# Kernel tuning notes

Hardware: AMD Instinct MI355X
Metric: run time of the kernel (lower is better)

The kernel has to match this reference:

```python
import jax, jax.numpy as jnp
import numpy as np

B, T = 64, 512
V, E, H, L = 100000, 256, 256, 9


def _lstm(x, Wx, Wh, b):
    # x: [B,T,E] -> hs: [B,T,H]; Keras gate order i,f,c,o
    xg = jnp.einsum('bte,eg->btg', x, Wx) + b  # [B,T,4H]
    h0 = jnp.zeros((x.shape[0], Wh.shape[0]), x.dtype)

    def step(carry, xt):
        h, c = carry
        g = xt + h @ Wh
        i, f, gc, o = jnp.split(g, 4, axis=-1)
        c = jax.nn.sigmoid(f) * c + jax.nn.sigmoid(i) * jnp.tanh(gc)
        h = jax.nn.sigmoid(o) * jnp.tanh(c)
        return (h, c), h

    _, hs = jax.lax.scan(step, (h0, h0), jnp.swapaxes(xg, 0, 1))
    return jnp.swapaxes(hs, 0, 1)


def _crf_log_likelihood(logits, tags, seq_len, trans):
    # logits: [B,T,L], tags: [B,T] int, seq_len: [B] int, trans: [L,L]
    Bb, Tt, Ll = logits.shape
    t_idx = jnp.arange(Tt)
    mask = (t_idx[None, :] < seq_len[:, None]).astype(logits.dtype)  # [B,T]
    # gold path score: unary + pairwise transitions
    unary = jnp.take_along_axis(logits, tags[..., None], axis=-1)[..., 0]  # [B,T]
    unary_score = jnp.sum(unary * mask, axis=-1)
    binary = trans[tags[:, :-1], tags[:, 1:]]  # [B,T-1]
    binary_score = jnp.sum(binary * mask[:, 1:], axis=-1)
    score = unary_score + binary_score
    # forward algorithm (log partition)
    alpha0 = logits[:, 0]  # [B,L]
    step_mask = t_idx[1:, None] < seq_len[None, :]  # [T-1,B]

    def step(alpha, xs):
        logit_t, m = xs  # [B,L], [B]
        new = jax.nn.logsumexp(alpha[:, :, None] + trans[None], axis=1) + logit_t
        alpha = jnp.where(m[:, None], new, alpha)
        return alpha, None

    alpha, _ = jax.lax.scan(step, alpha0, (jnp.swapaxes(logits[:, 1:], 0, 1), step_mask))
    log_norm = jax.nn.logsumexp(alpha, axis=-1)  # [B]
    return score - log_norm


def setup_inputs() -> dict:
    key = jax.random.key(0)
    ks = jax.random.split(key, 12)
    s = 0.05
    return {
        'tokens': jax.random.randint(ks[0], (B, T), 0, V),
        'labels': jax.random.randint(ks[1], (B, T), 0, L),
        'emb_table': jax.random.normal(ks[2], (V, E), jnp.float32) * s,
        'Wx_f': jax.random.normal(ks[3], (E, 4 * H), jnp.float32) * s,
        'Wh_f': jax.random.normal(ks[4], (H, 4 * H), jnp.float32) * s,
        'b_f': jnp.zeros((4 * H,), jnp.float32),
        'Wx_b': jax.random.normal(ks[5], (E, 4 * H), jnp.float32) * s,
        'Wh_b': jax.random.normal(ks[6], (H, 4 * H), jnp.float32) * s,
        'b_b': jnp.zeros((4 * H,), jnp.float32),
        'W_dense': jax.random.normal(ks[7], (2 * H, L), jnp.float32) * s,
        'b_dense': jnp.zeros((L,), jnp.float32),
        'trans': jax.random.uniform(ks[8], (L, L), jnp.float32),
    }


def reference(tokens, labels, emb_table, Wx_f, Wh_f, b_f, Wx_b, Wh_b, b_b, W_dense, b_dense, trans):
    # seq_len = count of non-pad (nonzero) tokens, as in the original call()
    seq_len = jnp.sum((tokens != 0).astype(jnp.int32), axis=-1)  # [B]
    emb = emb_table[tokens]  # [B,T,E]  (dropout inactive at inference)
    h_fwd = _lstm(emb, Wx_f, Wh_f, b_f)
    h_bwd = _lstm(emb[:, ::-1], Wx_b, Wh_b, b_b)[:, ::-1]
    enc = jnp.concatenate([h_fwd, h_bwd], axis=-1)  # [B,T,2H]
    logits = enc @ W_dense + b_dense  # [B,T,L]
    ll = _crf_log_likelihood(logits, labels, seq_len, trans)  # [B]
    return logits, seq_len, ll
```

## Files before the change

### kernel.cpp

```cpp
#include <hip/hip_runtime.h>
#include <hip/hip_fp16.h>


typedef unsigned int  uint32;
typedef unsigned short ushort16;
typedef unsigned long long uint64;
typedef __attribute__((ext_vector_type(8))) short  short8;
typedef __attribute__((ext_vector_type(4))) float  floatx4;
typedef __attribute__((ext_vector_type(2))) _Float16 half2t;

#define BB 64
#define TT 512
#define NT (BB*TT)
#define G4 1024
#define NL 9

__device__ inline float bf2f(ushort16 u) {
  return __builtin_bit_cast(float, ((uint32)u) << 16);
}
__device__ inline ushort16 f2bf(float f) {
  uint32 u = __builtin_bit_cast(uint32, f);
  u += 0x7fffu + ((u >> 16) & 1u);
  return (ushort16)(u >> 16);
}
__device__ inline float sigf(float x)  { return 1.0f / (1.0f + __expf(-x)); }
__device__ inline float tanhf_(float x){ return 1.0f - 2.0f / (1.0f + __expf(2.0f * x)); }

__device__ inline float fdot2_(uint32 w, half2t h, float acc) {
  return __builtin_amdgcn_fdot2(__builtin_bit_cast(half2t, w), h, acc, false);
}

__device__ inline void bar_lds() {
  __builtin_amdgcn_sched_barrier(0);
  asm volatile("s_waitcnt lgkmcnt(0)" ::: "memory");
  __builtin_amdgcn_s_barrier();
  __builtin_amdgcn_sched_barrier(0);
}

__global__ __launch_bounds__(64) void k_seqlen(const int* __restrict__ tokens,
                                               int* __restrict__ slen,
                                               float* __restrict__ out_sl) {
  const int b = blockIdx.x, lane = threadIdx.x;
  int cnt = 0;
  for (int t = lane; t < TT; t += 64) cnt += (tokens[b * TT + t] != 0) ? 1 : 0;
  #pragma unroll
  for (int off = 32; off >= 1; off >>= 1) cnt += __shfl_down(cnt, off, 64);
  if (lane == 0) { slen[b] = cnt; out_sl[b] = (float)cnt; }
}

__global__ __launch_bounds__(256) void k_embed(const int* __restrict__ tokens,
                                               const float* __restrict__ emb,
                                               ushort16* __restrict__ A) {
  const int f = blockIdx.x * 256 + threadIdx.x;
  const int e = f * 4;
  const int row = e >> 8;
  const int col = e & 255;
  const int tok = tokens[row];
  const float4 v = *(const float4*)(emb + (size_t)tok * 256 + col);
  uint32 lo = (uint32)f2bf(v.x) | ((uint32)f2bf(v.y) << 16);
  uint32 hi = (uint32)f2bf(v.z) | ((uint32)f2bf(v.w) << 16);
  *(uint2*)(A + e) = make_uint2(lo, hi);
}

__global__ __launch_bounds__(256) void k_wxprep(const float* __restrict__ Wxf,
                                                const float* __restrict__ Wxb,
                                                ushort16* __restrict__ BT) {
  const int id = blockIdx.x * 256 + threadIdx.x;
  const int c = id >> 8, k = id & 255;
  const float v = (c < G4) ? Wxf[k * G4 + c] : Wxb[k * G4 + (c - G4)];
  BT[c * 256 + k] = f2bf(v);
}

__global__ __launch_bounds__(256) void k_whprep(const float* __restrict__ Wh,
                                                uint32* __restrict__ W2) {
  const int id = blockIdx.x * 256 + threadIdx.x;
  const int k2 = id >> 10, c = id & 1023;
  const float w0 = Wh[(2 * k2) * G4 + c];
  const float w1 = Wh[(2 * k2 + 1) * G4 + c];
  const ushort16 b0 = __builtin_bit_cast(ushort16, (_Float16)w0);
  const ushort16 b1 = __builtin_bit_cast(ushort16, (_Float16)w1);
  W2[id] = ((uint32)b1 << 16) | (uint32)b0;
}

__global__ __launch_bounds__(256) void k_gemm_xg(const ushort16* __restrict__ A,
                                                 const ushort16* __restrict__ BT,
                                                 const float* __restrict__ bias_f,
                                                 const float* __restrict__ bias_b,
                                                 ushort16* __restrict__ xgf,
                                                 ushort16* __restrict__ xgb) {
  __shared__ __align__(16) ushort16 As[64 * 36];
  __shared__ __align__(16) ushort16 Bs[64 * 36];
  const int m0 = blockIdx.x * 64;
  const int n0 = blockIdx.y * 64;
  const int tid = threadIdx.x;
  const int wave = tid >> 6, lane = tid & 63;
  const int lr = tid >> 2;
  const int lc = (tid & 3) * 8;
  const int am = lane & 15, aq = lane >> 4;
  floatx4 acc[4];
  #pragma unroll
  for (int j = 0; j < 4; ++j) acc[j] = (floatx4){0.f, 0.f, 0.f, 0.f};

  for (int k0 = 0; k0 < 256; k0 += 32) {
    const uint4 va = *(const uint4*)(A  + ((m0 + lr) * 256 + k0 + lc));
    const uint4 vb = *(const uint4*)(BT + ((n0 + lr) * 256 + k0 + lc));
    *(uint2*)&As[lr * 36 + lc]     = make_uint2(va.x, va.y);
    *(uint2*)&As[lr * 36 + lc + 4] = make_uint2(va.z, va.w);
    *(uint2*)&Bs[lr * 36 + lc]     = make_uint2(vb.x, vb.y);
    *(uint2*)&Bs[lr * 36 + lc + 4] = make_uint2(vb.z, vb.w);
    __syncthreads();
    union { uint2 u[2]; short8 s; } fa, fb;
    fa.u[0] = *(const uint2*)&As[(wave * 16 + am) * 36 + aq * 8];
    fa.u[1] = *(const uint2*)&As[(wave * 16 + am) * 36 + aq * 8 + 4];
    #pragma unroll
    for (int j = 0; j < 4; ++j) {
      fb.u[0] = *(const uint2*)&Bs[(j * 16 + am) * 36 + aq * 8];
      fb.u[1] = *(const uint2*)&Bs[(j * 16 + am) * 36 + aq * 8 + 4];
      acc[j] = __builtin_amdgcn_mfma_f32_16x16x32_bf16(fa.s, fb.s, acc[j], 0, 0, 0);
    }
    __syncthreads();
  }
  const int orow = m0 + wave * 16 + aq * 4;
  #pragma unroll
  for (int j = 0; j < 4; ++j) {
    const int col = n0 + j * 16 + am;
    const float bv = (col < G4) ? bias_f[col] : bias_b[col - G4];
    #pragma unroll
    for (int r = 0; r < 4; ++r) {
      const float v = acc[j][r] + bv;
      const int row = orow + r;
      if (col < G4) xgf[row * G4 + col] = f2bf(v);
      else          xgb[row * G4 + (col - G4)] = f2bf(v);
    }
  }
}

__global__ __launch_bounds__(256) void k_zero(uint64* __restrict__ xh) {
  xh[blockIdx.x * 256 + threadIdx.x] = 0ull;
}

__global__ __launch_bounds__(1024, 1) void k_lstm(const ushort16* __restrict__ xgf,
                                                  const ushort16* __restrict__ xgb,
                                                  const uint32* __restrict__ Whf,
                                                  const uint32* __restrict__ Whb,
                                                  uint64* __restrict__ xh,
                                                  float* __restrict__ enc) {
  __shared__ __align__(16) uint32 h2[2][128];
  __shared__ float gl[512];
  __shared__ float glp[512];
  const int bid  = blockIdx.x;
  const int dir  = bid >> 7;
  const int b    = (bid >> 1) & 63;
  const int half = bid & 1;
  const int tid  = threadIdx.x;
  const int l    = tid & 63;
  const int c512 = tid & 511;
  const int q = c512 >> 7, r = c512 & 127;
  const int col = q * 256 + half * 128 + r;
  const bool ownk = (tid < 512);
  const ushort16* __restrict__ xg = dir ? xgb : xgf;
  const uint32* __restrict__ W2   = dir ? Whb : Whf;
  uint64* const xmine = xh + ((size_t)bid << 7);
  const uint64* const xpeer = xh + ((size_t)(bid ^ 1) << 7);

  const int rowbase = ownk ? (half * 64) : (64 - half * 64);
  uint32 wv[64];
  #pragma unroll
  for (int i = 0; i < 64; ++i) wv[i] = W2[(rowbase + i) * 1024 + col];
  #pragma unroll
  for (int i = 0; i < 64; ++i) asm volatile("" : "+v"(wv[i]));

  if (tid < 128) h2[0][tid] = 0u;
  float c_state = 0.f;
  __syncthreads();

  ushort16 xA = (ushort16)0;
  if (ownk) {
    const int t0 = dir ? (TT - 1) : 0;
    xA = xg[(size_t)(b * TT + t0) * G4 + col];
  }

#define HC(u) __builtin_bit_cast(half2t, u)
#define GR4(B,W) { const uint4 hq = hb[B]; \
                 a0 = fdot2_(wv[(W)*4+0], HC(hq.x), a0); \
                 a1 = fdot2_(wv[(W)*4+1], HC(hq.y), a1); \
                 a2 = fdot2_(wv[(W)*4+2], HC(hq.z), a2); \
                 a3 = fdot2_(wv[(W)*4+3], HC(hq.w), a3); }

  for (int s = 0; s < TT; ++s) {
    const int par = s & 1;
    float a0 = 0.f, a1 = 0.f, a2 = 0.f, a3 = 0.f;
    const uint4* hb = (const uint4*)h2[par];
    if (ownk) {
      a0 = bf2f(xA);
      if (s + 1 < TT) {
        const int t1 = dir ? (TT - 2 - s) : (s + 1);
        xA = xg[(size_t)(b * TT + t1) * G4 + col];
      }
      GR4(0,0)   GR4(1,1)   GR4(2,2)   GR4(3,3)
      GR4(4,4)   GR4(5,5)   GR4(6,6)   GR4(7,7)
      GR4(8,8)   GR4(9,9)   GR4(10,10) GR4(11,11)
      GR4(12,12) GR4(13,13) GR4(14,14) GR4(15,15)
    } else {
      if (s > 0) {
        const uint64* pp = xpeer + (par << 6) + l;
        const uint32 want = (uint32)s;
        uint64 pv = __hip_atomic_load(pp, __ATOMIC_RELAXED, __HIP_MEMORY_SCOPE_AGENT);
        while (!__all((uint32)(pv >> 32) == want)) {
          __builtin_amdgcn_s_sleep(1);
          pv = __hip_atomic_load(pp, __ATOMIC_RELAXED, __HIP_MEMORY_SCOPE_AGENT);
        }
        h2[par][64 + l] = (uint32)pv;
        __builtin_amdgcn_sched_barrier(0);
        asm volatile("s_waitcnt lgkmcnt(0)" ::: "memory");
        __builtin_amdgcn_sched_barrier(0);
      }
      GR4(16,0)  GR4(17,1)  GR4(18,2)  GR4(19,3)
      GR4(20,4)  GR4(21,5)  GR4(22,6)  GR4(23,7)
      GR4(24,8)  GR4(25,9)  GR4(26,10) GR4(27,11)
      GR4(28,12) GR4(29,13) GR4(30,14) GR4(31,15)
      glp[c512] = (a0 + a1) + (a2 + a3);
    }
    bar_lds();
    if (ownk) {
      float v = ((a0 + a1) + (a2 + a3)) + glp[c512];
      v = (q == 2) ? tanhf_(v) : sigf(v);
      gl[c512] = v;
    }
    bar_lds();
    if (tid < 128) {
      const float I = gl[tid];
      const float F = gl[128 + tid];
      const float G = gl[256 + tid];
      const float O = gl[384 + tid];
      c_state = F * c_state + I * G;
      const float h = O * tanhf_(c_state);
      const int hv = (int)(uint32)__builtin_bit_cast(ushort16, (_Float16)h);
      const int ho = __shfl_xor(hv, 1, 64);
      if (!(tid & 1)) {
        const uint32 pk = ((uint32)hv & 0xffffu) | ((uint32)ho << 16);
        if (s + 1 < TT) {
          const uint64 pv = ((uint64)(uint32)(s + 1) << 32) | (uint64)pk;
          __hip_atomic_store(xmine + ((par ^ 1) << 6) + (tid >> 1), pv,
                             __ATOMIC_RELAXED, __HIP_MEMORY_SCOPE_AGENT);
        }
        h2[par ^ 1][tid >> 1] = pk;
      }
      const int t = dir ? (TT - 1 - s) : s;
      enc[(size_t)(b * TT + t) * 512 + dir * 256 + half * 128 + tid] = h;
    }
    bar_lds();
  }
#undef HC
#undef GR4
}

__global__ __launch_bounds__(256) void k_dense(const float* __restrict__ enc,
                                               const float* __restrict__ Wd,
                                               const float* __restrict__ bd,
                                               float* __restrict__ logits) {
  __shared__ float Wl[512 * NL];
  __shared__ float bl[NL];
  const int tid = threadIdx.x;
  for (int i = tid; i < 512 * NL; i += 256) Wl[i] = Wd[i];
  if (tid < NL) bl[tid] = bd[tid];
  __syncthreads();
  const int wave = tid >> 6, lane = tid & 63;
  const int row = blockIdx.x * 4 + wave;
  const float* er = enc + (size_t)row * 512;
  float p[NL];
  #pragma unroll
  for (int c = 0; c < NL; ++c) p[c] = 0.f;
  #pragma unroll
  for (int u = 0; u < 8; ++u) {
    const int k = u * 64 + lane;
    const float v = er[k];
    const float* wr = &Wl[k * NL];
    #pragma unroll
    for (int c = 0; c < NL; ++c) p[c] += v * wr[c];
  }
  #pragma unroll
  for (int c = 0; c < NL; ++c) {
    #pragma unroll
    for (int off = 32; off >= 1; off >>= 1) p[c] += __shfl_down(p[c], off, 64);
  }
  if (lane == 0) {
    float* orow = logits + (size_t)row * NL;
    #pragma unroll
    for (int c = 0; c < NL; ++c) orow[c] = p[c] + bl[c];
  }
}

__global__ __launch_bounds__(64) void k_crf(const float* __restrict__ logits,
                                            const int* __restrict__ labels,
                                            const int* __restrict__ slen,
                                            const float* __restrict__ trans,
                                            float* __restrict__ out_ll) {
  __shared__ float tr[NL * NL];
  __shared__ float alpha[NL];
  const int b = blockIdx.x;
  const int lane = threadIdx.x;
  for (int i = lane; i < NL * NL; i += 64) tr[i] = trans[i];
  __syncthreads();
  const int len = slen[b];
  const int* tg = labels + b * TT;
  const float* lg = logits + (size_t)b * TT * NL;
  float s = 0.f;
  for (int t = lane; t < TT; t += 64)
    if (t < len) s += lg[t * NL + tg[t]];
  for (int t = lane; t < TT - 1; t += 64)
    if (t + 1 < len) s += tr[tg[t] * NL + tg[t + 1]];
  #pragma unroll
  for (int off = 32; off >= 1; off >>= 1) s += __shfl_down(s, off, 64);
  if (lane < NL) alpha[lane] = lg[lane];
  __syncthreads();
  if (lane < NL) {
    const int j = lane;
    for (int t = 1; t < TT; ++t) {
      if (t < len) {
        float av[NL];
        float m = -1e30f;
        #pragma unroll
        for (int i = 0; i < NL; ++i) { av[i] = alpha[i] + tr[i * NL + j]; m = fmaxf(m, av[i]); }
        float ss = 0.f;
        #pragma unroll
        for (int i = 0; i < NL; ++i) ss += __expf(av[i] - m);
        const float nj = m + __logf(ss) + lg[t * NL + j];
        alpha[j] = nj;
      }
    }
  }
  __syncthreads();
  if (lane == 0) {
    float m = -1e30f;
    #pragma unroll
    for (int i = 0; i < NL; ++i) m = fmaxf(m, alpha[i]);
    float ss = 0.f;
    #pragma unroll
    for (int i = 0; i < NL; ++i) ss += __expf(alpha[i] - m);
    out_ll[b] = s - (m + __logf(ss));
  }
}

extern "C" void kernel_launch(void* const* d_in, const int* in_sizes, int n_in,
                              void* d_out, int out_size, void* d_ws, size_t ws_size,
                              hipStream_t stream) {
  (void)in_sizes; (void)n_in; (void)out_size; (void)ws_size;
  const int*   tokens = (const int*)d_in[0];
  const int*   labels = (const int*)d_in[1];
  const float* emb    = (const float*)d_in[2];
  const float* Wxf    = (const float*)d_in[3];
  const float* Whf    = (const float*)d_in[4];
  const float* bf_    = (const float*)d_in[5];
  const float* Wxb    = (const float*)d_in[6];
  const float* Whb    = (const float*)d_in[7];
  const float* bb_    = (const float*)d_in[8];
  const float* Wd     = (const float*)d_in[9];
  const float* bd     = (const float*)d_in[10];
  const float* trans  = (const float*)d_in[11];
  float* out = (float*)d_out;

  char* ws = (char*)d_ws;
  ushort16* A    = (ushort16*)(ws + 0);
  ushort16* BT   = (ushort16*)(ws + 16777216);
  uint32*   W2f  = (uint32*)  (ws + 17825792);
  uint32*   W2b  = (uint32*)  (ws + 18350080);
  ushort16* xgf  = (ushort16*)(ws + 18874368);
  ushort16* xgb  = (ushort16*)(ws + 85983232);
  float*    enc  = (float*)   (ws + 153092096);
  int*      slen = (int*)     (ws + 220200960);
  uint64*   xh   = (uint64*)  (ws + 0);

  k_seqlen<<<BB, 64, 0, stream>>>(tokens, slen, out + NT * NL);
  k_embed <<<NT * 256 / 4 / 256, 256, 0, stream>>>(tokens, emb, A);
  k_wxprep<<<2048 * 256 / 256, 256, 0, stream>>>(Wxf, Wxb, BT);
  k_whprep<<<128 * 1024 / 256, 256, 0, stream>>>(Whf, W2f);
  k_whprep<<<128 * 1024 / 256, 256, 0, stream>>>(Whb, W2b);
  k_gemm_xg<<<dim3(NT / 64, 2048 / 64), 256, 0, stream>>>(A, BT, bf_, bb_, xgf, xgb);
  k_zero  <<<128, 256, 0, stream>>>(xh);
  k_lstm  <<<256, 1024, 0, stream>>>(xgf, xgb, W2f, W2b, xh, enc);
  k_dense <<<NT / 4, 256, 0, stream>>>(enc, Wd, bd, out);
  k_crf   <<<BB, 64, 0, stream>>>(out, labels, slen, trans, out + NT * NL + BB);
}
```

Baseline: 1.243 ms.

## Split K across both halves of the LSTM block to overlap peer wait

Every thread now computes half of its own-h dot product and half of its peer-h dot product, where before one half of the block handled own rows and the other half handled peer rows. Own-h work is issued before spinning on the peer's atomic flag, and the flag load is issued early, so the cross-block wait can overlap useful FMAs. Gate nonlinearities move into the 128-thread cell-update section, which removes one barrier per step but serialises four sigmoid/tanh per thread there. Peer pairing changes from bid^1 to bid^128, which alters block placement.

```diff
diff --git a/kernel.cpp b/kernel.cpp
--- a/kernel.cpp
+++ b/kernel.cpp
@@ -149,99 +149,102 @@
   __shared__ float gl[512];
   __shared__ float glp[512];
   const int bid  = blockIdx.x;
-  const int dir  = bid >> 7;
-  const int b    = (bid >> 1) & 63;
-  const int half = bid & 1;
+  const int seq  = bid & 127;
+  const int dir  = seq >> 6;
+  const int b    = seq & 63;
+  const int half = bid >> 7;
   const int tid  = threadIdx.x;
   const int l    = tid & 63;
   const int c512 = tid & 511;
+  const int kh   = tid >> 9;
+  const int kh8  = kh * 8;
   const int q = c512 >> 7, r = c512 & 127;
   const int col = q * 256 + half * 128 + r;
-  const bool ownk = (tid < 512);
   const ushort16* __restrict__ xg = dir ? xgb : xgf;
   const uint32* __restrict__ W2   = dir ? Whb : Whf;
   uint64* const xmine = xh + ((size_t)bid << 7);
-  const uint64* const xpeer = xh + ((size_t)(bid ^ 1) << 7);
-
-  const int rowbase = ownk ? (half * 64) : (64 - half * 64);
+  const uint64* const xpeer = xh + ((size_t)(bid ^ 128) << 7);
+
+  const int ownBase  = half * 64 + kh * 32;
+  const int peerBase = (64 - half * 64) + kh * 32;
   uint32 wv[64];
   #pragma unroll
-  for (int i = 0; i < 64; ++i) wv[i] = W2[(rowbase + i) * 1024 + col];
+  for (int i = 0; i < 32; ++i) wv[i]      = W2[(ownBase  + i) * 1024 + col];
+  #pragma unroll
+  for (int i = 0; i < 32; ++i) wv[32 + i] = W2[(peerBase + i) * 1024 + col];
   #pragma unroll
   for (int i = 0; i < 64; ++i) asm volatile("" : "+v"(wv[i]));
 
-  if (tid < 128) h2[0][tid] = 0u;
+  if (tid < 256) h2[tid >> 7][tid & 127] = 0u;
   float c_state = 0.f;
   __syncthreads();
 
   ushort16 xA = (ushort16)0;
-  if (ownk) {
+  if (kh == 0) {
     const int t0 = dir ? (TT - 1) : 0;
     xA = xg[(size_t)(b * TT + t0) * G4 + col];
   }
 
 #define HC(u) __builtin_bit_cast(half2t, u)
-#define GR4(B,W) { const uint4 hq = hb[B]; \
-                 a0 = fdot2_(wv[(W)*4+0], HC(hq.x), a0); \
-                 a1 = fdot2_(wv[(W)*4+1], HC(hq.y), a1); \
-                 a2 = fdot2_(wv[(W)*4+2], HC(hq.z), a2); \
-                 a3 = fdot2_(wv[(W)*4+3], HC(hq.w), a3); }
+#define GRO(J) { const uint4 hq = hb[kh8 + (J)]; \
+                 a0 = fdot2_(wv[(J)*4+0], HC(hq.x), a0); \
+                 a1 = fdot2_(wv[(J)*4+1], HC(hq.y), a1); \
+                 a2 = fdot2_(wv[(J)*4+2], HC(hq.z), a2); \
+                 a3 = fdot2_(wv[(J)*4+3], HC(hq.w), a3); }
+#define GRP(J) { const uint4 hq = hb[16 + kh8 + (J)]; \
+                 a0 = fdot2_(wv[32+(J)*4+0], HC(hq.x), a0); \
+                 a1 = fdot2_(wv[32+(J)*4+1], HC(hq.y), a1); \
+                 a2 = fdot2_(wv[32+(J)*4+2], HC(hq.z), a2); \
+                 a3 = fdot2_(wv[32+(J)*4+3], HC(hq.w), a3); }
 
   for (int s = 0; s < TT; ++s) {
     const int par = s & 1;
     float a0 = 0.f, a1 = 0.f, a2 = 0.f, a3 = 0.f;
-    const uint4* hb = (const uint4*)h2[par];
-    if (ownk) {
+    const uint64* pp = xpeer + (par << 6) + l;
+    uint64 pv = 0;
+    if (s > 0)
+      pv = __hip_atomic_load(pp, __ATOMIC_RELAXED, __HIP_MEMORY_SCOPE_AGENT);
+    if (kh == 0) {
       a0 = bf2f(xA);
       if (s + 1 < TT) {
         const int t1 = dir ? (TT - 2 - s) : (s + 1);
         xA = xg[(size_t)(b * TT + t1) * G4 + col];
       }
-      GR4(0,0)   GR4(1,1)   GR4(2,2)   GR4(3,3)
-      GR4(4,4)   GR4(5,5)   GR4(6,6)   GR4(7,7)
-      GR4(8,8)   GR4(9,9)   GR4(10,10) GR4(11,11)
-      GR4(12,12) GR4(13,13) GR4(14,14) GR4(15,15)
-    } else {
-      if (s > 0) {
-        const uint64* pp = xpeer + (par << 6) + l;
-        const uint32 want = (uint32)s;
-        uint64 pv = __hip_atomic_load(pp, __ATOMIC_RELAXED, __HIP_MEMORY_SCOPE_AGENT);
-        while (!__all((uint32)(pv >> 32) == want)) {
-          __builtin_amdgcn_s_sleep(1);
-          pv = __hip_atomic_load(pp, __ATOMIC_RELAXED, __HIP_MEMORY_SCOPE_AGENT);
-        }
-        h2[par][64 + l] = (uint32)pv;
-        __builtin_amdgcn_sched_barrier(0);
-        asm volatile("s_waitcnt lgkmcnt(0)" ::: "memory");
-        __builtin_amdgcn_sched_barrier(0);
+    }
+    __builtin_amdgcn_sched_barrier(0);
+    const uint4* hb = (const uint4*)h2[par];
+    GRO(0) GRO(1) GRO(2) GRO(3) GRO(4) GRO(5) GRO(6) GRO(7)
+    if (s > 0) {
+      const uint32 want = (uint32)s;
+      while (!__all((uint32)(pv >> 32) == want)) {
+        __builtin_amdgcn_s_sleep(1);
+        pv = __hip_atomic_load(pp, __ATOMIC_RELAXED, __HIP_MEMORY_SCOPE_AGENT);
       }
-      GR4(16,0)  GR4(17,1)  GR4(18,2)  GR4(19,3)
-      GR4(20,4)  GR4(21,5)  GR4(22,6)  GR4(23,7)
-      GR4(24,8)  GR4(25,9)  GR4(26,10) GR4(27,11)
-      GR4(28,12) GR4(29,13) GR4(30,14) GR4(31,15)
-      glp[c512] = (a0 + a1) + (a2 + a3);
-    }
-    bar_lds();
-    if (ownk) {
-      float v = ((a0 + a1) + (a2 + a3)) + glp[c512];
-      v = (q == 2) ? tanhf_(v) : sigf(v);
-      gl[c512] = v;
+      h2[par][64 + l] = (uint32)pv;
+      __builtin_amdgcn_sched_barrier(0);
+      asm volatile("s_waitcnt lgkmcnt(0)" ::: "memory");
+      __builtin_amdgcn_sched_barrier(0);
+    }
+    GRP(0) GRP(1) GRP(2) GRP(3) GRP(4) GRP(5) GRP(6) GRP(7)
+    {
+      const float v = (a0 + a1) + (a2 + a3);
+      if (kh == 0) gl[c512] = v; else glp[c512] = v;
     }
     bar_lds();
     if (tid < 128) {
-      const float I = gl[tid];
-      const float F = gl[128 + tid];
-      const float G = gl[256 + tid];
-      const float O = gl[384 + tid];
-      c_state = F * c_state + I * G;
-      const float h = O * tanhf_(c_state);
+      const float Ir = gl[tid]       + glp[tid];
+      const float Fr = gl[128 + tid] + glp[128 + tid];
+      const float Gr = gl[256 + tid] + glp[256 + tid];
+      const float Or = gl[384 + tid] + glp[384 + tid];
+      c_state = sigf(Fr) * c_state + sigf(Ir) * tanhf_(Gr);
+      const float h = sigf(Or) * tanhf_(c_state);
       const int hv = (int)(uint32)__builtin_bit_cast(ushort16, (_Float16)h);
       const int ho = __shfl_xor(hv, 1, 64);
       if (!(tid & 1)) {
         const uint32 pk = ((uint32)hv & 0xffffu) | ((uint32)ho << 16);
         if (s + 1 < TT) {
-          const uint64 pv = ((uint64)(uint32)(s + 1) << 32) | (uint64)pk;
-          __hip_atomic_store(xmine + ((par ^ 1) << 6) + (tid >> 1), pv,
+          const uint64 pvo = ((uint64)(uint32)(s + 1) << 32) | (uint64)pk;
+          __hip_atomic_store(xmine + ((par ^ 1) << 6) + (tid >> 1), pvo,
                              __ATOMIC_RELAXED, __HIP_MEMORY_SCOPE_AGENT);
         }
         h2[par ^ 1][tid >> 1] = pk;
@@ -252,7 +255,8 @@
     bar_lds();
   }
 #undef HC
-#undef GR4
+#undef GRO
+#undef GRP
 }
 
 __global__ __launch_bounds__(256) void k_dense(const float* __restrict__ enc,
```

Result: slower. 1.348 ms (+8.4%).
